# Optimization experiments

Hardware: AMD Instinct MI355X
Metric: run time of the kernel (lower is better)

Reference implementation:

```python
import jax, jax.numpy as jnp
import numpy as np
import math

HEAD_DIM = 64
N_HEADS = 64
N_KV = 8
HIDDEN = 2880
BASE = 150000.0
INIT_CTX = 4096
SCALING = 32.0
NTK_ALPHA = 1.0
NTK_BETA = 32.0
SM_SCALE = 1.0 / math.sqrt(HEAD_DIM)
EPS = 1e-5


def _rope_cos_sin(T):
    # YaRN-scaled rotary frequencies (see RotaryEmbedding._compute_concentration_and_inv_freq)
    freq = BASE ** (jnp.arange(0, HEAD_DIM, 2, dtype=jnp.float32) / HEAD_DIM)
    concentration = 0.1 * math.log(SCALING) + 1.0
    d_half = HEAD_DIM / 2
    low = d_half * math.log(INIT_CTX / (NTK_BETA * 2 * math.pi)) / math.log(BASE)
    high = d_half * math.log(INIT_CTX / (NTK_ALPHA * 2 * math.pi)) / math.log(BASE)
    interp = 1.0 / (SCALING * freq)
    extrap = 1.0 / freq
    ramp = (jnp.arange(d_half, dtype=jnp.float32) - low) / (high - low)
    mask = 1.0 - jnp.clip(ramp, 0.0, 1.0)
    inv_freq = interp * (1.0 - mask) + extrap * mask
    tpos = jnp.arange(T, dtype=jnp.float32)
    freqs = jnp.outer(tpos, inv_freq)            # [T, HEAD_DIM/2]
    return jnp.cos(freqs) * concentration, jnp.sin(freqs) * concentration


def _apply_rotary(x, cos, sin):
    # x: [T, H, D]; cos/sin: [T, D/2]
    cos = cos[:, None, :]
    sin = sin[:, None, :]
    x1, x2 = jnp.split(x, 2, axis=-1)
    return jnp.concatenate([x1 * cos - x2 * sin, x2 * cos + x1 * sin], axis=-1)


def setup_inputs() -> dict:
    key = jax.random.key(0)
    ks = jax.random.split(key, 4)
    T = 2048
    qkv_dim = HEAD_DIM * (N_HEADS + 2 * N_KV)   # 4608
    x = jax.random.normal(ks[0], (T, HIDDEN), jnp.float32)
    norm_scale = jnp.ones((HIDDEN,), jnp.float32)
    qkv_w = jax.random.normal(ks[1], (qkv_dim, HIDDEN), jnp.float32) * 0.02
    qkv_b = jnp.zeros((qkv_dim,), jnp.float32)
    out_w = jax.random.normal(ks[2], (HIDDEN, N_HEADS * HEAD_DIM), jnp.float32) * 0.02
    out_b = jnp.zeros((HIDDEN,), jnp.float32)
    return {"x": x, "norm_scale": norm_scale, "qkv_w": qkv_w, "qkv_b": qkv_b,
            "out_w": out_w, "out_b": out_b}


def reference(x, norm_scale, qkv_w, qkv_b, out_w, out_b):
    T = x.shape[0]
    # RMSNorm (computed in fp32, as in the torch module)
    t = x * jax.lax.rsqrt(jnp.mean(x * x, axis=-1, keepdims=True) + EPS) * norm_scale
    # Fused QKV projection
    qkv = t @ qkv_w.T + qkv_b                    # [T, 4608]
    qd = N_HEADS * HEAD_DIM
    kd = N_KV * HEAD_DIM
    q = qkv[:, :qd].reshape(T, N_HEADS, HEAD_DIM)
    k = qkv[:, qd:qd + kd].reshape(T, N_KV, HEAD_DIM)
    v = qkv[:, qd + kd:qd + 2 * kd].reshape(T, N_KV, HEAD_DIM)
    # YaRN RoPE
    cos, sin = _rope_cos_sin(T)
    q = _apply_rotary(q, cos, sin)
    k = _apply_rotary(k, cos, sin)
    # GQA causal attention (cache=None path: sinks ignored, full causal mask)
    qmult = N_HEADS // N_KV
    q = q.reshape(T, N_KV, qmult, HEAD_DIM)      # [T, g, m, d]
    scores = jnp.einsum('qgmd,kgd->gmqk', q, k) * SM_SCALE  # [g, m, T, T]
    causal = jnp.arange(T)[:, None] >= jnp.arange(T)[None, :]
    scores = jnp.where(causal[None, None], scores, -jnp.inf)
    attn = jax.nn.softmax(scores, axis=-1)
    o = jnp.einsum('gmqk,kgd->qgmd', attn, v).reshape(T, N_HEADS * HEAD_DIM)
    # Output projection + residual
    return o @ out_w.T + out_b + x
```

## Files before the change

kernel.cpp:

```cpp
#include <hip/hip_runtime.h>
#include <stdint.h>
#include <math.h>

#define T_SEQ 2048
#define HID   2880
#define QKV_D 5120
#define OD    4096
#define NQH   64
#define SM_SCALE 0.125f
#define LOG2E 1.44269504088896340736f
#define SSL (SM_SCALE * LOG2E)

typedef float f32x4 __attribute__((ext_vector_type(4)));
typedef float f32x16 __attribute__((ext_vector_type(16)));
typedef short bf16x8 __attribute__((ext_vector_type(8)));

__device__ __forceinline__ unsigned short f2bf(float f) {
  union { float f; unsigned u; } v; v.f = f;
  unsigned r = v.u + 0x7fffu + ((v.u >> 16) & 1u);
  return (unsigned short)(r >> 16);
}
__device__ __forceinline__ float bf2f(unsigned short h) {
  union { unsigned u; float f; } v; v.u = ((unsigned)h) << 16;
  return v.f;
}
__device__ __forceinline__ void gld_lds16(const void* g, void* l) {
  __builtin_amdgcn_global_load_lds(
      (const __attribute__((address_space(1))) unsigned int*)g,
      (__attribute__((address_space(3))) unsigned int*)l, 16, 0, 0);
}

__global__ __launch_bounds__(256) void rmsnorm_k(const float* __restrict__ x,
                                                 const float* __restrict__ scale,
                                                 unsigned short* __restrict__ t) {
  int row = blockIdx.x;
  const float4* xr = (const float4*)(x + (size_t)row * HID);
  float s = 0.f;
  for (int i = threadIdx.x; i < 720; i += 256) {
    float4 a = xr[i];
    s += a.x * a.x + a.y * a.y + a.z * a.z + a.w * a.w;
  }
#pragma unroll
  for (int off = 32; off; off >>= 1) s += __shfl_down(s, off);
  __shared__ float wsum[4];
  int w = threadIdx.x >> 6, lane = threadIdx.x & 63;
  if (lane == 0) wsum[w] = s;
  __syncthreads();
  float tot = wsum[0] + wsum[1] + wsum[2] + wsum[3];
  float r = rsqrtf(tot / (float)HID + 1e-5f);
  const float4* sc4 = (const float4*)scale;
  ushort4* tr = (ushort4*)(t + (size_t)row * HID);
  for (int i = threadIdx.x; i < 720; i += 256) {
    float4 a = xr[i]; float4 b = sc4[i];
    ushort4 o;
    o.x = f2bf(a.x * r * b.x); o.y = f2bf(a.y * r * b.y);
    o.z = f2bf(a.z * r * b.z); o.w = f2bf(a.w * r * b.w);
    tr[i] = o;
  }
}

__global__ __launch_bounds__(256) void f2bf_k(const float* __restrict__ in,
                                              unsigned short* __restrict__ out, int n4) {
  int i = blockIdx.x * 256 + threadIdx.x;
  int stride = gridDim.x * 256;
  for (; i < n4; i += stride) {
    float4 a = ((const float4*)in)[i];
    ushort4 o;
    o.x = f2bf(a.x); o.y = f2bf(a.y); o.z = f2bf(a.z); o.w = f2bf(a.w);
    ((ushort4*)out)[i] = o;
  }
}

__global__ __launch_bounds__(256) void rope_tab_k(float* __restrict__ ct, float* __restrict__ st) {
  int idx = blockIdx.x * 256 + threadIdx.x;
  int i = idx & 31, t = idx >> 5;
  double fi = (double)i;
  double freq = pow(150000.0, fi / 32.0);
  double lb = log(150000.0);
  double low  = 32.0 * log(4096.0 / (32.0 * 2.0 * M_PI)) / lb;
  double high = 32.0 * log(4096.0 / (1.0  * 2.0 * M_PI)) / lb;
  double interp = 1.0 / (32.0 * freq);
  double extrap = 1.0 / freq;
  double ramp = (fi - low) / (high - low);
  ramp = fmin(fmax(ramp, 0.0), 1.0);
  double mask = 1.0 - ramp;
  double invf = interp * (1.0 - mask) + extrap * mask;
  double conc = 0.1 * log(32.0) + 1.0;
  double th = (double)t * invf;
  ct[idx] = (float)(cos(th) * conc);
  st[idx] = (float)(sin(th) * conc);
}

__global__ __launch_bounds__(256) void rope_apply_k(unsigned short* __restrict__ qkv,
                                                    const float* __restrict__ ct,
                                                    const float* __restrict__ st) {
  int idx = blockIdx.x * 256 + threadIdx.x;
  int i = idx & 31;
  int hh = (idx >> 5) % 72;
  int t = idx / (72 * 32);
  size_t base = (size_t)t * QKV_D + hh * 64 + i;
  float x1 = bf2f(qkv[base]), x2 = bf2f(qkv[base + 32]);
  float c = ct[t * 32 + i], s = st[t * 32 + i];
  qkv[base]      = f2bf(x1 * c - x2 * s);
  qkv[base + 32] = f2bf(x2 * c + x1 * s);
}

__global__ __launch_bounds__(256) void vtrans_k(const unsigned short* __restrict__ qkv,
                                                unsigned short* __restrict__ vt) {
  __shared__ unsigned short tile[64][72];
  int g = blockIdx.y;
  int t0 = blockIdx.x * 64;
  int tid = threadIdx.x;
#pragma unroll
  for (int p = 0; p < 2; ++p) {
    int ch = p * 256 + tid;
    int i = ch >> 3, j0 = (ch & 7) * 8;
    bf16x8 v = *(const bf16x8*)(qkv + (size_t)(t0 + i) * QKV_D + 4608 + g * 64 + j0);
    *(bf16x8*)&tile[i][j0] = v;
  }
  __syncthreads();
#pragma unroll
  for (int p = 0; p < 2; ++p) {
    int ch = p * 256 + tid;
    int j = ch >> 3, i0 = (ch & 7) * 8;
    union { unsigned short u[8]; bf16x8 v; } pk;
#pragma unroll
    for (int m = 0; m < 8; ++m) pk.u[m] = tile[i0 + m][j];
    *(bf16x8*)(vt + (size_t)(g * 64 + j) * T_SEQ + t0 + i0) = pk.v;
  }
}

template <bool FINAL>
__global__ __launch_bounds__(512, 4) void gemm8_k(const unsigned short* __restrict__ A,
                                                  const unsigned short* __restrict__ B,
                                                  const float* __restrict__ bias,
                                                  const float* __restrict__ resid,
                                                  unsigned short* __restrict__ Cb,
                                                  float* __restrict__ Cf,
                                                  int M, int N, int K) {
  __shared__ unsigned short As[2][128 * 32];
  __shared__ unsigned short Bs[2][128 * 32];
  int tid = threadIdx.x;
  int w = tid >> 6, lane = tid & 63;
  int g = lane >> 4, ln = lane & 15;
  int nwg = gridDim.x * gridDim.y;
  int lin = blockIdx.y * gridDim.x + blockIdx.x;
  int swz = (lin & 7) * (nwg >> 3) + (lin >> 3);
  int bx = swz % gridDim.x, by = swz / gridDim.x;
  int m0 = by * 128, n0 = bx * 128;
  int wr = w >> 1, wc = w & 1;
  f32x4 acc[2][4];
#pragma unroll
  for (int a = 0; a < 2; a++)
#pragma unroll
    for (int b = 0; b < 4; b++) acc[a][b] = (f32x4){0.f, 0.f, 0.f, 0.f};

  int srow = tid >> 2, scc = tid & 3;
  int sg = scc ^ (srow & 3);
  const unsigned short* gA = A + (size_t)(m0 + srow) * K + sg * 8;
  int rowB = n0 + srow; if (rowB > N - 1) rowB = N - 1;
  const unsigned short* gB = B + (size_t)rowB * K + sg * 8;

  int nt = K >> 5;
  gld_lds16(gA, &As[0][(w * 64) * 8]);
  gld_lds16(gB, &Bs[0][(w * 64) * 8]);
  __syncthreads();
  int cur = 0;
  for (int t = 0; t < nt; ++t) {
    if (t + 1 < nt) {
      int k0 = (t + 1) << 5;
      gld_lds16(gA + k0, &As[cur ^ 1][(w * 64) * 8]);
      gld_lds16(gB + k0, &Bs[cur ^ 1][(w * 64) * 8]);
    }
    bf16x8 af[2], bfr[4];
#pragma unroll
    for (int mi = 0; mi < 2; ++mi) {
      int rm = wr * 32 + mi * 16 + ln;
      int c = g ^ (rm & 3);
      af[mi] = *(const bf16x8*)&As[cur][rm * 32 + c * 8];
    }
#pragma unroll
    for (int ni = 0; ni < 4; ++ni) {
      int rn = wc * 64 + ni * 16 + ln;
      int c = g ^ (rn & 3);
      bfr[ni] = *(const bf16x8*)&Bs[cur][rn * 32 + c * 8];
    }
#pragma unroll
    for (int mi = 0; mi < 2; ++mi)
#pragma unroll
      for (int ni = 0; ni < 4; ++ni)
        acc[mi][ni] = __builtin_amdgcn_mfma_f32_16x16x32_bf16(af[mi], bfr[ni], acc[mi][ni], 0, 0, 0);
    __syncthreads();
    cur ^= 1;
  }
#pragma unroll
  for (int mi = 0; mi < 2; ++mi)
#pragma unroll
    for (int ni = 0; ni < 4; ++ni) {
      int colB = n0 + wc * 64 + ni * 16 + ln;
      if (colB >= N) continue;
      float bv = bias[colB];
#pragma unroll
      for (int r = 0; r < 4; ++r) {
        int rowC = m0 + wr * 32 + mi * 16 + g * 4 + r;
        float v = acc[mi][ni][r] + bv;
        if (FINAL) {
          Cf[(size_t)rowC * N + colB] = v + resid[(size_t)rowC * N + colB];
        } else {
          Cb[(size_t)rowC * N + colB] = f2bf(v);
        }
      }
    }
}

__global__ __launch_bounds__(256) void attn2_k(const unsigned short* __restrict__ qkv,
                                               const unsigned short* __restrict__ vt,
                                               unsigned short* __restrict__ o) {
  __shared__ unsigned short Ks[2][64 * 64];
  __shared__ unsigned short Vs[2][64 * 64];
  int h = blockIdx.x;
  int qt = (int)gridDim.y - 1 - (int)blockIdx.y;
  int tid = threadIdx.x;
  int w = tid >> 6, lane = tid & 63;
  int l31 = lane & 31, hi = lane >> 5;
  int qb0 = qt * 128;
  int q0w = qb0 + w * 32;
  int kvh = h >> 3;
  const unsigned short* kbase = qkv + 4096 + (size_t)kvh * 64;
  const unsigned short* vtb = vt + (size_t)kvh * 64 * T_SEQ;

  bf16x8 qf[4];
  {
    const unsigned short* qrow = qkv + (size_t)(q0w + l31) * QKV_D + h * 64;
#pragma unroll
    for (int dt = 0; dt < 4; ++dt)
      qf[dt] = *(const bf16x8*)(qrow + dt * 16 + hi * 8);
  }
  f32x16 oacc[2];
#pragma unroll
  for (int r = 0; r < 16; ++r) { oacc[0][r] = 0.f; oacc[1][r] = 0.f; }
  float m_run = -1e30f, l_run = 0.f;
  int nt = qt * 2 + 2;

  auto STAGE = [&](int t, int buf) {
    int kv0 = t * 64;
#pragma unroll
    for (int p = 0; p < 2; ++p) {
      int ch = p * 256 + w * 64 + lane;
      int row = ch >> 3, cc = ch & 7;
      int gch = cc ^ (row & 7);
      gld_lds16(kbase + (size_t)(kv0 + row) * QKV_D + gch * 8, &Ks[buf][(p * 256 + w * 64) * 8]);
      gld_lds16(vtb + (size_t)row * T_SEQ + kv0 + gch * 8, &Vs[buf][(p * 256 + w * 64) * 8]);
    }
  };

  STAGE(0, 0);
  __syncthreads();
  for (int t = 0; t < nt; ++t) {
    int cur = t & 1;
    if (t + 1 < nt) STAGE(t + 1, cur ^ 1);
    int kv0 = t * 64;
    if (kv0 <= q0w + 31) {
      const unsigned short* K_ = Ks[cur];
      const unsigned short* V_ = Vs[cur];
      f32x16 pa[2];
#pragma unroll
      for (int kt2 = 0; kt2 < 2; ++kt2) {
        f32x16 acc;
#pragma unroll
        for (int r = 0; r < 16; ++r) acc[r] = 0.f;
        int rk = kt2 * 32 + l31;
#pragma unroll
        for (int dt = 0; dt < 4; ++dt) {
          int c = dt * 2 + hi;
          bf16x8 kf = *(const bf16x8*)&K_[rk * 64 + (c ^ (rk & 7)) * 8];
          acc = __builtin_amdgcn_mfma_f32_32x32x16_bf16(kf, qf[dt], acc, 0, 0, 0);
        }
        pa[kt2] = acc;
      }
      bool diag = (kv0 + 64 > q0w);
      int q = q0w + l31;
      float s2[32];
#pragma unroll
      for (int kt2 = 0; kt2 < 2; ++kt2)
#pragma unroll
        for (int r = 0; r < 16; ++r) {
          float x = pa[kt2][r] * SSL;
          if (diag) {
            int k = kv0 + kt2 * 32 + (r & 3) + 8 * (r >> 2) + 4 * hi;
            if (k > q) x = -3.0e38f;
          }
          s2[kt2 * 16 + r] = x;
        }
      float mx = s2[0];
#pragma unroll
      for (int i = 1; i < 32; ++i) mx = fmaxf(mx, s2[i]);
      mx = fmaxf(mx, __shfl_xor(mx, 32));
      float mnew = fmaxf(m_run, mx);
      float alpha = exp2f(m_run - mnew);
      m_run = mnew;
      float sum = 0.f;
#pragma unroll
      for (int i = 0; i < 32; ++i) {
        float p = exp2f(s2[i] - mnew);
        s2[i] = p;
        sum += p;
      }
      sum += __shfl_xor(sum, 32);
      l_run = l_run * alpha + sum;
#pragma unroll
      for (int r = 0; r < 16; ++r) { oacc[0][r] *= alpha; oacc[1][r] *= alpha; }
      unsigned pw[16];
#pragma unroll
      for (int kt2 = 0; kt2 < 2; ++kt2)
#pragma unroll
        for (int i = 0; i < 8; ++i) {
          unsigned r_;
          asm("v_cvt_pk_bf16_f32 %0, %1, %2"
              : "=v"(r_) : "v"(s2[kt2 * 16 + 2 * i]), "v"(s2[kt2 * 16 + 2 * i + 1]));
          pw[kt2 * 8 + i] = r_;
        }
      unsigned bw[2][2][4];
#pragma unroll
      for (int kt2 = 0; kt2 < 2; ++kt2)
#pragma unroll
        for (int a = 0; a < 2; ++a) {
          unsigned p0 = pw[kt2 * 8 + a * 4 + 0];
          unsigned p1 = pw[kt2 * 8 + a * 4 + 1];
          unsigned p2 = pw[kt2 * 8 + a * 4 + 2];
          unsigned p3 = pw[kt2 * 8 + a * 4 + 3];
          unsigned e0 = (unsigned)__shfl_xor((int)p0, 32);
          unsigned e1 = (unsigned)__shfl_xor((int)p1, 32);
          unsigned e2 = (unsigned)__shfl_xor((int)p2, 32);
          unsigned e3 = (unsigned)__shfl_xor((int)p3, 32);
          bw[kt2][a][0] = hi ? e2 : p0;
          bw[kt2][a][1] = hi ? e3 : p1;
          bw[kt2][a][2] = hi ? p2 : e0;
          bw[kt2][a][3] = hi ? p3 : e1;
        }
#pragma unroll
      for (int db = 0; db < 2; ++db) {
        f32x16 acc = oacc[db];
        int rd = db * 32 + l31;
#pragma unroll
        for (int kt2 = 0; kt2 < 2; ++kt2)
#pragma unroll
          for (int a = 0; a < 2; ++a) {
            int c = kt2 * 4 + a * 2 + hi;
            bf16x8 vf = *(const bf16x8*)&V_[rd * 64 + (c ^ (rd & 7)) * 8];
            union { unsigned u[4]; bf16x8 v; } pun;
            pun.u[0] = bw[kt2][a][0]; pun.u[1] = bw[kt2][a][1];
            pun.u[2] = bw[kt2][a][2]; pun.u[3] = bw[kt2][a][3];
            acc = __builtin_amdgcn_mfma_f32_32x32x16_bf16(vf, pun.v, acc, 0, 0, 0);
          }
        oacc[db] = acc;
      }
    }
    __syncthreads();
  }
  float inv = 1.f / l_run;
  int q = q0w + l31;
#pragma unroll
  for (int db = 0; db < 2; ++db)
#pragma unroll
    for (int r = 0; r < 16; r += 2) {
      int d = db * 32 + (r & 3) + 8 * (r >> 2) + 4 * hi;
      unsigned short lo_ = f2bf(oacc[db][r] * inv);
      unsigned short hi_ = f2bf(oacc[db][r + 1] * inv);
      unsigned u = (unsigned)lo_ | ((unsigned)hi_ << 16);
      *(unsigned*)(o + (size_t)q * OD + h * 64 + d) = u;
    }
}

extern "C" void kernel_launch(void* const* d_in, const int* in_sizes, int n_in,
                              void* d_out, int out_size, void* d_ws, size_t ws_size,
                              hipStream_t stream) {
  const float* x          = (const float*)d_in[0];
  const float* norm_scale = (const float*)d_in[1];
  const float* qkv_w      = (const float*)d_in[2];
  const float* qkv_b      = (const float*)d_in[3];
  const float* out_w      = (const float*)d_in[4];
  const float* out_b      = (const float*)d_in[5];
  float* out = (float*)d_out;

  char* ws = (char*)d_ws;
  size_t off = 0;
  auto alloc = [&](size_t bytes) {
    void* p = ws + off;
    off += (bytes + 255) & ~(size_t)255;
    return p;
  };
  unsigned short* t_bf = (unsigned short*)alloc((size_t)T_SEQ * HID * 2);
  unsigned short* wqkv = (unsigned short*)alloc((size_t)QKV_D * HID * 2);
  unsigned short* wout = (unsigned short*)alloc((size_t)HID * OD * 2);
  unsigned short* qkv  = (unsigned short*)alloc((size_t)T_SEQ * QKV_D * 2);
  unsigned short* obuf = (unsigned short*)alloc((size_t)T_SEQ * OD * 2);
  unsigned short* vtb  = (unsigned short*)alloc((size_t)8 * 64 * T_SEQ * 2);
  float* ct = (float*)alloc((size_t)T_SEQ * 32 * 4);
  float* st = (float*)alloc((size_t)T_SEQ * 32 * 4);

  rmsnorm_k<<<dim3(T_SEQ), dim3(256), 0, stream>>>(x, norm_scale, t_bf);
  f2bf_k<<<dim3(1024), dim3(256), 0, stream>>>(qkv_w, wqkv, QKV_D * HID / 4);
  f2bf_k<<<dim3(1024), dim3(256), 0, stream>>>(out_w, wout, HID * OD / 4);
  rope_tab_k<<<dim3(T_SEQ * 32 / 256), dim3(256), 0, stream>>>(ct, st);
  gemm8_k<false><<<dim3(QKV_D / 128, T_SEQ / 128), dim3(512), 0, stream>>>(
      t_bf, wqkv, qkv_b, nullptr, qkv, nullptr, T_SEQ, QKV_D, HID);
  rope_apply_k<<<dim3(T_SEQ * 72 * 32 / 256), dim3(256), 0, stream>>>(qkv, ct, st);
  vtrans_k<<<dim3(T_SEQ / 64, 8), dim3(256), 0, stream>>>(qkv, vtb);
  attn2_k<<<dim3(NQH, T_SEQ / 128), dim3(256), 0, stream>>>(qkv, vtb, obuf);
  gemm8_k<true><<<dim3((HID + 127) / 128, T_SEQ / 128), dim3(512), 0, stream>>>(
      obuf, wout, out_b, x, nullptr, out, T_SEQ, HID, OD);
}
```

Baseline: 426.8 us.

## Restructure attention inner loop with lazy rescale, permlane swap, and priority hints

The attention kernel's KV loop is unrolled by two with fixed LDS buffers and pointer-increment staging, which removes per-iteration index arithmetic. Softmax now computes the max on raw scores and folds the scale into an FMA before exp2. It skips the output rescale unless the running max grows by more than 8 (log2 domain). The shuffle-based P transpose is replaced with v_permlane32_swap, and s_setprio is raised around the MFMA sections to favour matrix work across waves. The lazy-rescale threshold loosens the numeric bounds on intermediate values, and the unroll assumes nt is even.

```diff
diff --git a/kernel.cpp b/kernel.cpp
--- a/kernel.cpp
+++ b/kernel.cpp
@@ -213,6 +213,9 @@
     }
 }
 
+#define MAX8(V, B) fmaxf(fmaxf(fmaxf((V)[B], (V)[B + 1]), fmaxf((V)[B + 2], (V)[B + 3])), \
+                         fmaxf(fmaxf((V)[B + 4], (V)[B + 5]), fmaxf((V)[B + 6], (V)[B + 7])))
+
 __global__ __launch_bounds__(256) void attn2_k(const unsigned short* __restrict__ qkv,
                                                const unsigned short* __restrict__ vt,
                                                unsigned short* __restrict__ o) {
@@ -241,125 +244,133 @@
   for (int r = 0; r < 16; ++r) { oacc[0][r] = 0.f; oacc[1][r] = 0.f; }
   float m_run = -1e30f, l_run = 0.f;
   int nt = qt * 2 + 2;
-
-  auto STAGE = [&](int t, int buf) {
-    int kv0 = t * 64;
-#pragma unroll
-    for (int p = 0; p < 2; ++p) {
-      int ch = p * 256 + w * 64 + lane;
-      int row = ch >> 3, cc = ch & 7;
-      int gch = cc ^ (row & 7);
-      gld_lds16(kbase + (size_t)(kv0 + row) * QKV_D + gch * 8, &Ks[buf][(p * 256 + w * 64) * 8]);
-      gld_lds16(vtb + (size_t)row * T_SEQ + kv0 + gch * 8, &Vs[buf][(p * 256 + w * 64) * 8]);
-    }
+  int q = q0w + l31;
+
+  int ch = w * 64 + lane;
+  int srow = ch >> 3, scc = ch & 7;
+  int sgch = scc ^ (srow & 7);
+  const unsigned short* gk  = kbase + (size_t)srow * QKV_D + sgch * 8;
+  const unsigned short* gk2 = gk + (size_t)32 * QKV_D;
+  const unsigned short* gv  = vtb + (size_t)srow * T_SEQ + sgch * 8;
+  const unsigned short* gv2 = gv + (size_t)32 * T_SEQ;
+
+  auto STAGE = [&](int buf) {
+    unsigned short* Kd = &Ks[buf][0];
+    unsigned short* Vd = &Vs[buf][0];
+    gld_lds16(gk,  Kd + (w * 64) * 8);
+    gld_lds16(gk2, Kd + (256 + w * 64) * 8);
+    gld_lds16(gv,  Vd + (w * 64) * 8);
+    gld_lds16(gv2, Vd + (256 + w * 64) * 8);
+    gk += 64 * QKV_D; gk2 += 64 * QKV_D;
+    gv += 64; gv2 += 64;
   };
 
-  STAGE(0, 0);
-  __syncthreads();
-  for (int t = 0; t < nt; ++t) {
-    int cur = t & 1;
-    if (t + 1 < nt) STAGE(t + 1, cur ^ 1);
-    int kv0 = t * 64;
-    if (kv0 <= q0w + 31) {
-      const unsigned short* K_ = Ks[cur];
-      const unsigned short* V_ = Vs[cur];
-      f32x16 pa[2];
-#pragma unroll
-      for (int kt2 = 0; kt2 < 2; ++kt2) {
-        f32x16 acc;
-#pragma unroll
-        for (int r = 0; r < 16; ++r) acc[r] = 0.f;
-        int rk = kt2 * 32 + l31;
-#pragma unroll
-        for (int dt = 0; dt < 4; ++dt) {
-          int c = dt * 2 + hi;
-          bf16x8 kf = *(const bf16x8*)&K_[rk * 64 + (c ^ (rk & 7)) * 8];
-          acc = __builtin_amdgcn_mfma_f32_32x32x16_bf16(kf, qf[dt], acc, 0, 0, 0);
+  auto COMPUTE = [&](const unsigned short* K_, const unsigned short* V_, int kv0) {
+    f32x16 pa[2];
+    __builtin_amdgcn_s_setprio(1);
+#pragma unroll
+    for (int kt2 = 0; kt2 < 2; ++kt2) {
+      f32x16 acc;
+#pragma unroll
+      for (int r = 0; r < 16; ++r) acc[r] = 0.f;
+      int rk = kt2 * 32 + l31;
+#pragma unroll
+      for (int dt = 0; dt < 4; ++dt) {
+        int c = dt * 2 + hi;
+        bf16x8 kf = *(const bf16x8*)&K_[rk * 64 + (c ^ (rk & 7)) * 8];
+        acc = __builtin_amdgcn_mfma_f32_32x32x16_bf16(kf, qf[dt], acc, 0, 0, 0);
+      }
+      pa[kt2] = acc;
+    }
+    __builtin_amdgcn_s_setprio(0);
+    if (kv0 + 64 > q0w) {
+#pragma unroll
+      for (int kt2 = 0; kt2 < 2; ++kt2)
+#pragma unroll
+        for (int r = 0; r < 16; ++r) {
+          int k = kv0 + kt2 * 32 + (r & 3) + 8 * (r >> 2) + 4 * hi;
+          pa[kt2][r] = (k > q) ? -3.0e38f : pa[kt2][r];
         }
-        pa[kt2] = acc;
-      }
-      bool diag = (kv0 + 64 > q0w);
-      int q = q0w + l31;
-      float s2[32];
-#pragma unroll
-      for (int kt2 = 0; kt2 < 2; ++kt2)
-#pragma unroll
-        for (int r = 0; r < 16; ++r) {
-          float x = pa[kt2][r] * SSL;
-          if (diag) {
-            int k = kv0 + kt2 * 32 + (r & 3) + 8 * (r >> 2) + 4 * hi;
-            if (k > q) x = -3.0e38f;
-          }
-          s2[kt2 * 16 + r] = x;
-        }
-      float mx = s2[0];
-#pragma unroll
-      for (int i = 1; i < 32; ++i) mx = fmaxf(mx, s2[i]);
-      mx = fmaxf(mx, __shfl_xor(mx, 32));
-      float mnew = fmaxf(m_run, mx);
+    }
+    float mx = fmaxf(fmaxf(MAX8(pa[0], 0), MAX8(pa[0], 8)),
+                     fmaxf(MAX8(pa[1], 0), MAX8(pa[1], 8)));
+    mx = fmaxf(mx, __shfl_xor(mx, 32));
+    float mxs = mx * SSL;
+    if (!__all(mxs <= m_run + 8.f)) {
+      float mnew = fmaxf(m_run, mxs);
       float alpha = exp2f(m_run - mnew);
       m_run = mnew;
-      float sum = 0.f;
-#pragma unroll
-      for (int i = 0; i < 32; ++i) {
-        float p = exp2f(s2[i] - mnew);
-        s2[i] = p;
-        sum += p;
+      l_run *= alpha;
+#pragma unroll
+      for (int r = 0; r < 16; ++r) { oacc[0][r] *= alpha; oacc[1][r] *= alpha; }
+    }
+    float negm = -m_run;
+    float sa[4] = {0.f, 0.f, 0.f, 0.f};
+#pragma unroll
+    for (int kt2 = 0; kt2 < 2; ++kt2)
+#pragma unroll
+      for (int r = 0; r < 16; ++r) {
+        float p = exp2f(fmaf(pa[kt2][r], SSL, negm));
+        pa[kt2][r] = p;
+        sa[r & 3] += p;
       }
-      sum += __shfl_xor(sum, 32);
-      l_run = l_run * alpha + sum;
-#pragma unroll
-      for (int r = 0; r < 16; ++r) { oacc[0][r] *= alpha; oacc[1][r] *= alpha; }
-      unsigned pw[16];
+    float sum = (sa[0] + sa[1]) + (sa[2] + sa[3]);
+    sum += __shfl_xor(sum, 32);
+    l_run += sum;
+    unsigned pw[16];
+#pragma unroll
+    for (int kt2 = 0; kt2 < 2; ++kt2)
+#pragma unroll
+      for (int i = 0; i < 8; ++i) {
+        unsigned r_;
+        asm("v_cvt_pk_bf16_f32 %0, %1, %2"
+            : "=v"(r_) : "v"(pa[kt2][2 * i]), "v"(pa[kt2][2 * i + 1]));
+        pw[kt2 * 8 + i] = r_;
+      }
+    unsigned bw[2][2][4];
+#pragma unroll
+    for (int kt2 = 0; kt2 < 2; ++kt2)
+#pragma unroll
+      for (int a = 0; a < 2; ++a) {
+        unsigned x0 = pw[kt2 * 8 + a * 4 + 0], y0 = pw[kt2 * 8 + a * 4 + 2];
+        asm volatile("v_permlane32_swap_b32 %0, %1" : "+v"(x0), "+v"(y0));
+        unsigned x1 = pw[kt2 * 8 + a * 4 + 1], y1 = pw[kt2 * 8 + a * 4 + 3];
+        asm volatile("v_permlane32_swap_b32 %0, %1" : "+v"(x1), "+v"(y1));
+        bw[kt2][a][0] = x0; bw[kt2][a][2] = y0;
+        bw[kt2][a][1] = x1; bw[kt2][a][3] = y1;
+      }
+    __builtin_amdgcn_s_setprio(1);
+#pragma unroll
+    for (int db = 0; db < 2; ++db) {
+      f32x16 acc = oacc[db];
+      int rd = db * 32 + l31;
 #pragma unroll
       for (int kt2 = 0; kt2 < 2; ++kt2)
 #pragma unroll
-        for (int i = 0; i < 8; ++i) {
-          unsigned r_;
-          asm("v_cvt_pk_bf16_f32 %0, %1, %2"
-              : "=v"(r_) : "v"(s2[kt2 * 16 + 2 * i]), "v"(s2[kt2 * 16 + 2 * i + 1]));
-          pw[kt2 * 8 + i] = r_;
+        for (int a = 0; a < 2; ++a) {
+          int c = kt2 * 4 + a * 2 + hi;
+          bf16x8 vf = *(const bf16x8*)&V_[rd * 64 + (c ^ (rd & 7)) * 8];
+          union { unsigned u[4]; bf16x8 v; } pun;
+          pun.u[0] = bw[kt2][a][0]; pun.u[1] = bw[kt2][a][1];
+          pun.u[2] = bw[kt2][a][2]; pun.u[3] = bw[kt2][a][3];
+          acc = __builtin_amdgcn_mfma_f32_32x32x16_bf16(vf, pun.v, acc, 0, 0, 0);
         }
-      unsigned bw[2][2][4];
-#pragma unroll
-      for (int kt2 = 0; kt2 < 2; ++kt2)
-#pragma unroll
-        for (int a = 0; a < 2; ++a) {
-          unsigned p0 = pw[kt2 * 8 + a * 4 + 0];
-          unsigned p1 = pw[kt2 * 8 + a * 4 + 1];
-          unsigned p2 = pw[kt2 * 8 + a * 4 + 2];
-          unsigned p3 = pw[kt2 * 8 + a * 4 + 3];
-          unsigned e0 = (unsigned)__shfl_xor((int)p0, 32);
-          unsigned e1 = (unsigned)__shfl_xor((int)p1, 32);
-          unsigned e2 = (unsigned)__shfl_xor((int)p2, 32);
-          unsigned e3 = (unsigned)__shfl_xor((int)p3, 32);
-          bw[kt2][a][0] = hi ? e2 : p0;
-          bw[kt2][a][1] = hi ? e3 : p1;
-          bw[kt2][a][2] = hi ? p2 : e0;
-          bw[kt2][a][3] = hi ? p3 : e1;
-        }
-#pragma unroll
-      for (int db = 0; db < 2; ++db) {
-        f32x16 acc = oacc[db];
-        int rd = db * 32 + l31;
-#pragma unroll
-        for (int kt2 = 0; kt2 < 2; ++kt2)
-#pragma unroll
-          for (int a = 0; a < 2; ++a) {
-            int c = kt2 * 4 + a * 2 + hi;
-            bf16x8 vf = *(const bf16x8*)&V_[rd * 64 + (c ^ (rd & 7)) * 8];
-            union { unsigned u[4]; bf16x8 v; } pun;
-            pun.u[0] = bw[kt2][a][0]; pun.u[1] = bw[kt2][a][1];
-            pun.u[2] = bw[kt2][a][2]; pun.u[3] = bw[kt2][a][3];
-            acc = __builtin_amdgcn_mfma_f32_32x32x16_bf16(vf, pun.v, acc, 0, 0, 0);
-          }
-        oacc[db] = acc;
-      }
-    }
+      oacc[db] = acc;
+    }
+    __builtin_amdgcn_s_setprio(0);
+  };
+
+  STAGE(0);
+  __syncthreads();
+  for (int t = 0; t < nt; t += 2) {
+    STAGE(1);
+    if (t * 64 <= q0w + 31) COMPUTE(Ks[0], Vs[0], t * 64);
     __syncthreads();
+    if (t + 2 < nt) STAGE(0);
+    if ((t + 1) * 64 <= q0w + 31) COMPUTE(Ks[1], Vs[1], (t + 1) * 64);
+    __syncthreads();
   }
   float inv = 1.f / l_run;
-  int q = q0w + l31;
 #pragma unroll
   for (int db = 0; db < 2; ++db)
 #pragma unroll
```

Result: slower. 435.6 us (+2.1%).
